# Optimization experiments

Hardware: AMD Instinct MI355X
Metric: run time of the kernel (lower is better)

## Reference

```python
import jax, jax.numpy as jnp
import numpy as np

N = 102400          # total nodes
G = 64              # graphs
S = 16              # subgraphs per graph
NODES_PER_SG = 100  # nodes per subgraph (N = G*S*NODES_PER_SG)
D = 128             # in_dim == emb_dim
L = 5               # num_layer
E = 819200          # edges (avg degree 8)
TOTAL_SG = G * S    # total subgraphs = 1024 (static)


def setup_inputs() -> dict:
    key = jax.random.key(0)
    kx, ke, kw1, kw2, keps = jax.random.split(key, 5)
    x = jax.random.normal(kx, (N, D), dtype=jnp.float32)
    edge_index = jax.random.randint(ke, (2, E), 0, N, dtype=jnp.int32)
    # node -> graph id (contiguous blocks of S*NODES_PER_SG nodes)
    batch = (jnp.arange(N, dtype=jnp.int32) // (S * NODES_PER_SG)).astype(jnp.int32)
    # node -> local subgraph id within its graph
    subgraph_batch = ((jnp.arange(N, dtype=jnp.int32) // NODES_PER_SG) % S).astype(jnp.int32)
    num_subgraphs = jnp.full((G,), S, dtype=jnp.int32)
    # GIN MLP params per layer: Linear(D,2D) -> ReLU -> Linear(2D,D)
    s1 = 1.0 / np.sqrt(D)
    s2 = 1.0 / np.sqrt(2 * D)
    W1 = jax.random.normal(kw1, (L, D, 2 * D), dtype=jnp.float32) * s1
    b1 = jnp.zeros((L, 2 * D), dtype=jnp.float32)
    W2 = jax.random.normal(kw2, (L, 2 * D, D), dtype=jnp.float32) * s2
    b2 = jnp.zeros((L, D), dtype=jnp.float32)
    eps = jnp.zeros((L,), dtype=jnp.float32)
    return {"x": x, "edge_index": edge_index, "batch": batch,
            "subgraph_batch": subgraph_batch, "num_subgraphs": num_subgraphs,
            "W1": W1, "b1": b1, "W2": W2, "b2": b2, "eps": eps}


def reference(x, edge_index, batch, subgraph_batch, num_subgraphs, W1, b1, W2, b2, eps):
    src, dst = edge_index[0], edge_index[1]
    n = x.shape[0]
    h = x
    for i in range(L):
        # GIN aggregation: (1+eps)*h + sum over incoming messages
        agg = jax.ops.segment_sum(h[src], dst, num_segments=n)
        z = (1.0 + eps[i]) * h + agg
        z = jax.nn.relu(z @ W1[i] + b1[i]) @ W2[i] + b2[i]
        h = z if i == L - 1 else jax.nn.relu(z)  # inter-layer ReLU, JK='last'
    # subgraph_pool: global subgraph index = graph offset + local subgraph id
    tmp = jnp.concatenate([jnp.zeros((1,), num_subgraphs.dtype),
                           jnp.cumsum(num_subgraphs)])
    subgraph_idx = tmp[batch] + subgraph_batch  # [N], values in [0, TOTAL_SG)
    sums = jax.ops.segment_sum(h, subgraph_idx, num_segments=TOTAL_SG)
    cnt = jax.ops.segment_sum(jnp.ones((n, 1), h.dtype), subgraph_idx,
                              num_segments=TOTAL_SG)
    return sums / jnp.maximum(cnt, 1.0)  # global_mean_pool over subgraphs
```

## Files before the change

kernel.cpp:

```cpp
#include <hip/hip_runtime.h>
#include <cstddef>

#define NN   102400
#define D    128
#define D2   256
#define NE   819200
#define NL   5
#define NSG  1024
#define SGN  100

typedef __attribute__((ext_vector_type(8))) short short8;
typedef __attribute__((ext_vector_type(4))) float f32x4;

__device__ __forceinline__ float bf2f(unsigned short u) {
  union { unsigned int i; float f; } c; c.i = ((unsigned int)u) << 16; return c.f;
}
__device__ __forceinline__ unsigned short f2bf(float f) {
  union { float f; unsigned int i; } c; c.f = f;
  unsigned int x = c.i;
  return (unsigned short)((x + 0x7fffu + ((x >> 16) & 1u)) >> 16);
}

__global__ void k_count(const int* __restrict__ dst, int* __restrict__ deg,
                        int* __restrict__ rank) {
  int e = blockIdx.x * blockDim.x + threadIdx.x;
  if (e < NE) rank[e] = atomicAdd(&deg[dst[e]], 1);
}

__global__ void k_scan_local(const int* __restrict__ deg, int* __restrict__ incl,
                             int* __restrict__ part) {
  __shared__ int s[1024];
  int i = blockIdx.x * 1024 + threadIdx.x;
  s[threadIdx.x] = deg[i];
  __syncthreads();
  for (int off = 1; off < 1024; off <<= 1) {
    int t = (threadIdx.x >= off) ? s[threadIdx.x - off] : 0;
    __syncthreads();
    s[threadIdx.x] += t;
    __syncthreads();
  }
  incl[i] = s[threadIdx.x];
  if (threadIdx.x == 1023) part[blockIdx.x] = s[1023];
}

__global__ void k_scan_part(int* part, int nb) {
  if (threadIdx.x == 0 && blockIdx.x == 0) {
    int acc = 0;
    for (int i = 0; i < nb; ++i) { int t = part[i]; part[i] = acc; acc += t; }
  }
}

__global__ void k_scan_fin(const int* __restrict__ incl, const int* __restrict__ part,
                           int* __restrict__ rowptr) {
  int i = blockIdx.x * blockDim.x + threadIdx.x;
  if (i < NN) rowptr[i + 1] = incl[i] + part[i >> 10];
  if (i == 0) rowptr[0] = 0;
}

__global__ void k_fill(const int* __restrict__ src, const int* __restrict__ dst,
                       const int* __restrict__ rowptr, const int* __restrict__ rank,
                       int* __restrict__ csrsrc) {
  int e = blockIdx.x * blockDim.x + threadIdx.x;
  if (e < NE) csrsrc[rowptr[dst[e]] + rank[e]] = src[e];
}

__global__ void k_cvt_x(const float* __restrict__ x, unsigned short* __restrict__ xb) {
  int i = blockIdx.x * 256 + threadIdx.x;
  const float* p = x + (size_t)i * 8;
  float4 a = *(const float4*)p;
  float4 b = *(const float4*)(p + 4);
  short8 o;
  o[0] = (short)f2bf(a.x); o[1] = (short)f2bf(a.y);
  o[2] = (short)f2bf(a.z); o[3] = (short)f2bf(a.w);
  o[4] = (short)f2bf(b.x); o[5] = (short)f2bf(b.y);
  o[6] = (short)f2bf(b.z); o[7] = (short)f2bf(b.w);
  *(short8*)(xb + (size_t)i * 8) = o;
}

__global__ void k_prep_w(const float* __restrict__ W1, const float* __restrict__ W2,
                         unsigned short* __restrict__ W1t, unsigned short* __restrict__ W2t) {
  int i = blockIdx.x * 256 + threadIdx.x;
  int l = i >> 15;
  int rem = i & 32767;
  int n1 = rem >> 7, k1 = rem & 127;
  W1t[i] = f2bf(W1[(size_t)l * D * D2 + (size_t)k1 * D2 + n1]);
  int n2 = rem >> 8, k2 = rem & 255;
  W2t[i] = f2bf(W2[(size_t)l * D2 * D + (size_t)k2 * D + n2]);
}

template<bool RELU_OUT>
__global__ __launch_bounds__(256, 2) void k_layer(
    const unsigned short* __restrict__ hin, const int* __restrict__ rowptr,
    const int* __restrict__ csrsrc,
    const unsigned short* __restrict__ W1t,
    const float* __restrict__ b1,
    const unsigned short* __restrict__ W2t,
    const float* __restrict__ b2,
    const float* __restrict__ eps, int layer,
    unsigned short* __restrict__ hout) {
  __shared__ char lds[4 * 4096];
  int w = threadIdx.x >> 6, lane = threadIdx.x & 63;
  int l15 = lane & 15, q = lane >> 4;
  char* my = lds + w * 4096;
  float ep1 = 1.0f + eps[layer];
  int rowA = blockIdx.x * 128 + w * 32;

  short8 azf[2][4];
#pragma unroll
  for (int m = 0; m < 2; ++m) {
    int r = rowA + m * 16 + l15;
    const unsigned short* hr = hin + (size_t)r * D + q * 8;
    float acc[4][8];
#pragma unroll
    for (int kf = 0; kf < 4; ++kf) {
      short8 v = *(const short8*)(hr + kf * 32);
#pragma unroll
      for (int j = 0; j < 8; ++j) acc[kf][j] = ep1 * bf2f((unsigned short)v[j]);
    }
    int e0 = rowptr[r], e1 = rowptr[r + 1];
    for (int e = e0; e < e1; ++e) {
      int u = csrsrc[e];
      const unsigned short* hu = hin + (size_t)u * D + q * 8;
#pragma unroll
      for (int kf = 0; kf < 4; ++kf) {
        short8 v = *(const short8*)(hu + kf * 32);
#pragma unroll
        for (int j = 0; j < 8; ++j) acc[kf][j] += bf2f((unsigned short)v[j]);
      }
    }
#pragma unroll
    for (int kf = 0; kf < 4; ++kf) {
      short8 o;
#pragma unroll
      for (int j = 0; j < 8; ++j) o[j] = (short)f2bf(acc[kf][j]);
      azf[m][kf] = o;
    }
  }

  f32x4 acc2[2][8] = {};
#pragma unroll
  for (int nc = 0; nc < 4; ++nc) {
    f32x4 acc1[2][4] = {};
#pragma unroll
    for (int kf = 0; kf < 4; ++kf) {
#pragma unroll
      for (int n = 0; n < 4; ++n) {
        int col = nc * 64 + n * 16 + l15;
        short8 bf = *(const short8*)(W1t + (size_t)col * D + kf * 32 + q * 8);
        acc1[0][n] = __builtin_amdgcn_mfma_f32_16x16x32_bf16(azf[0][kf], bf, acc1[0][n], 0, 0, 0);
        acc1[1][n] = __builtin_amdgcn_mfma_f32_16x16x32_bf16(azf[1][kf], bf, acc1[1][n], 0, 0, 0);
      }
    }
#pragma unroll
    for (int m = 0; m < 2; ++m) {
#pragma unroll
      for (int n = 0; n < 4; ++n) {
        int cc = n * 16 + l15;
        float bb = b1[nc * 64 + cc];
#pragma unroll
        for (int r = 0; r < 4; ++r) {
          int rs = m * 16 + q * 4 + r;
          float v = fmaxf(acc1[m][n][r] + bb, 0.f);
          int byte = (rs << 7) + cc * 2;
          byte ^= (rs & 7) << 4;
          *(unsigned short*)(my + byte) = f2bf(v);
        }
      }
    }
#pragma unroll
    for (int kk = 0; kk < 2; ++kk) {
      short8 af[2];
#pragma unroll
      for (int m = 0; m < 2; ++m) {
        int rs = m * 16 + l15;
        int byte = (rs << 7) + kk * 64 + q * 16;
        byte ^= (rs & 7) << 4;
        af[m] = *(const short8*)(my + byte);
      }
#pragma unroll
      for (int n2 = 0; n2 < 8; ++n2) {
        short8 bf = *(const short8*)(W2t + (size_t)(n2 * 16 + l15) * D2 +
                                     nc * 64 + kk * 32 + q * 8);
        acc2[0][n2] = __builtin_amdgcn_mfma_f32_16x16x32_bf16(af[0], bf, acc2[0][n2], 0, 0, 0);
        acc2[1][n2] = __builtin_amdgcn_mfma_f32_16x16x32_bf16(af[1], bf, acc2[1][n2], 0, 0, 0);
      }
    }
  }

#pragma unroll
  for (int m = 0; m < 2; ++m) {
#pragma unroll
    for (int n2 = 0; n2 < 8; ++n2) {
      int col = n2 * 16 + l15;
      float bb = b2[col];
#pragma unroll
      for (int r = 0; r < 4; ++r) {
        int row = rowA + m * 16 + q * 4 + r;
        float v = acc2[m][n2][r] + bb;
        if (RELU_OUT) v = fmaxf(v, 0.f);
        hout[(size_t)row * D + col] = f2bf(v);
      }
    }
  }
}

__global__ __launch_bounds__(256) void k_pool(const unsigned short* __restrict__ h,
                                              float* __restrict__ out) {
  __shared__ float red[16][132];
  int g = threadIdx.x >> 4;
  int ln = threadIdx.x & 15;
  int sg = blockIdx.x;
  float acc[8] = {0.f, 0.f, 0.f, 0.f, 0.f, 0.f, 0.f, 0.f};
  for (int r = g; r < SGN; r += 16) {
    short8 v = *(const short8*)(h + ((size_t)sg * SGN + r) * D + (size_t)ln * 8);
#pragma unroll
    for (int j = 0; j < 8; ++j) acc[j] += bf2f((unsigned short)v[j]);
  }
#pragma unroll
  for (int j = 0; j < 8; ++j) red[g][ln * 8 + j] = acc[j];
  __syncthreads();
  if (threadIdx.x < 128) {
    float s = 0.f;
#pragma unroll
    for (int i = 0; i < 16; ++i) s += red[i][threadIdx.x];
    out[(size_t)sg * D + threadIdx.x] = s * 0.01f;
  }
}

extern "C" void kernel_launch(void* const* d_in, const int* in_sizes, int n_in,
                              void* d_out, int out_size, void* d_ws, size_t ws_size,
                              hipStream_t stream) {
  const float* x   = (const float*)d_in[0];
  const int*   ei  = (const int*)d_in[1];
  const float* W1  = (const float*)d_in[5];
  const float* b1  = (const float*)d_in[6];
  const float* W2  = (const float*)d_in[7];
  const float* b2  = (const float*)d_in[8];
  const float* eps = (const float*)d_in[9];
  const int* src = ei;
  const int* dst = ei + NE;

  char* p = (char*)d_ws;
  unsigned short* xb  = (unsigned short*)p; p += (size_t)NN * D * 2;
  unsigned short* hb  = (unsigned short*)p; p += (size_t)NN * D * 2;
  unsigned short* zb  = (unsigned short*)p; p += (size_t)NN * D * 2;
  unsigned short* W1t = (unsigned short*)p; p += (size_t)NL * D * D2 * 2;
  unsigned short* W2t = (unsigned short*)p; p += (size_t)NL * D * D2 * 2;
  int* deg    = (int*)p;   p += (size_t)NN * 4;
  int* incl   = (int*)p;   p += (size_t)NN * 4;
  int* part   = (int*)p;   p += 128 * 4;
  int* rowptr = (int*)p;   p += (size_t)(NN + 1) * 4;
  int* rank   = (int*)p;   p += (size_t)NE * 4;
  int* csrsrc = (int*)p;   p += (size_t)NE * 4;

  hipMemsetAsync(deg, 0, (size_t)NN * 4, stream);
  k_count<<<NE / 256, 256, 0, stream>>>(dst, deg, rank);
  k_scan_local<<<NN / 1024, 1024, 0, stream>>>(deg, incl, part);
  k_scan_part<<<1, 64, 0, stream>>>(part, NN / 1024);
  k_scan_fin<<<NN / 256, 256, 0, stream>>>(incl, part, rowptr);
  k_fill<<<NE / 256, 256, 0, stream>>>(src, dst, rowptr, rank, csrsrc);

  k_cvt_x<<<NN * D / 8 / 256, 256, 0, stream>>>(x, xb);
  k_prep_w<<<NL * D * D2 / 256, 256, 0, stream>>>(W1, W2, W1t, W2t);

  const unsigned short* cur = xb;
  unsigned short* nxt = hb;
  for (int l = 0; l < NL; ++l) {
    const unsigned short* w1l = W1t + (size_t)l * D * D2;
    const unsigned short* w2l = W2t + (size_t)l * D * D2;
    const float* b1l = b1 + (size_t)l * D2;
    const float* b2l = b2 + (size_t)l * D;
    if (l < NL - 1)
      k_layer<true><<<NN / 128, 256, 0, stream>>>(cur, rowptr, csrsrc, w1l, b1l,
                                                  w2l, b2l, eps, l, nxt);
    else
      k_layer<false><<<NN / 128, 256, 0, stream>>>(cur, rowptr, csrsrc, w1l, b1l,
                                                   w2l, b2l, eps, l, nxt);
    cur = nxt;
    nxt = (cur == hb) ? zb : hb;
  }
  k_pool<<<NSG, 256, 0, stream>>>((const unsigned short*)cur, (float*)d_out);
}
```

Before: 745.6 us.

## Split neighbor aggregation into a separate high-parallelism kernel before the MLP

Neighbor aggregation moves out of the fused layer kernel into its own kernel. Each node gets 16 threads, one 16-byte slice each, and the edge loop is unrolled by four so more gathers are in flight. The MLP kernel then just loads the aggregated bf16 rows. This is meant to fix the poor memory-level parallelism of the fused gather, where the MFMA-oriented thread layout and the register pressure of launch_bounds(256,2) limited outstanding loads. In exchange it adds an extra write and read of an N×D bf16 buffer per layer plus one extra launch per layer.

```diff
diff --git a/kernel.cpp b/kernel.cpp
--- a/kernel.cpp
+++ b/kernel.cpp
@@ -88,54 +88,67 @@
   W2t[i] = f2bf(W2[(size_t)l * D2 * D + (size_t)k2 * D + n2]);
 }
 
+__global__ __launch_bounds__(256) void k_agg(const unsigned short* __restrict__ h,
+                                             const int* __restrict__ rowptr,
+                                             const int* __restrict__ csrsrc,
+                                             const float* __restrict__ eps, int layer,
+                                             unsigned short* __restrict__ z) {
+  int g = threadIdx.x >> 4;
+  int ln = threadIdx.x & 15;
+  int v = blockIdx.x * 16 + g;
+  float ep1 = 1.0f + eps[layer];
+  const size_t off = (size_t)ln * 8;
+
+  short8 hv = *(const short8*)(h + (size_t)v * D + off);
+  float acc[8];
+#pragma unroll
+  for (int j = 0; j < 8; ++j) acc[j] = ep1 * bf2f((unsigned short)hv[j]);
+
+  int e = rowptr[v], r1 = rowptr[v + 1];
+  for (; e + 3 < r1; e += 4) {
+    int u0 = csrsrc[e], u1 = csrsrc[e + 1], u2 = csrsrc[e + 2], u3 = csrsrc[e + 3];
+    short8 a = *(const short8*)(h + (size_t)u0 * D + off);
+    short8 b = *(const short8*)(h + (size_t)u1 * D + off);
+    short8 c = *(const short8*)(h + (size_t)u2 * D + off);
+    short8 d = *(const short8*)(h + (size_t)u3 * D + off);
+#pragma unroll
+    for (int j = 0; j < 8; ++j)
+      acc[j] += (bf2f((unsigned short)a[j]) + bf2f((unsigned short)b[j])) +
+                (bf2f((unsigned short)c[j]) + bf2f((unsigned short)d[j]));
+  }
+  for (; e < r1; ++e) {
+    int u0 = csrsrc[e];
+    short8 a = *(const short8*)(h + (size_t)u0 * D + off);
+#pragma unroll
+    for (int j = 0; j < 8; ++j) acc[j] += bf2f((unsigned short)a[j]);
+  }
+
+  short8 o;
+#pragma unroll
+  for (int j = 0; j < 8; ++j) o[j] = (short)f2bf(acc[j]);
+  *(short8*)(z + (size_t)v * D + off) = o;
+}
+
 template<bool RELU_OUT>
-__global__ __launch_bounds__(256, 2) void k_layer(
-    const unsigned short* __restrict__ hin, const int* __restrict__ rowptr,
-    const int* __restrict__ csrsrc,
+__global__ __launch_bounds__(256, 2) void k_mlp(
+    const unsigned short* __restrict__ z,
     const unsigned short* __restrict__ W1t,
     const float* __restrict__ b1,
     const unsigned short* __restrict__ W2t,
     const float* __restrict__ b2,
-    const float* __restrict__ eps, int layer,
     unsigned short* __restrict__ hout) {
   __shared__ char lds[4 * 4096];
   int w = threadIdx.x >> 6, lane = threadIdx.x & 63;
   int l15 = lane & 15, q = lane >> 4;
   char* my = lds + w * 4096;
-  float ep1 = 1.0f + eps[layer];
   int rowA = blockIdx.x * 128 + w * 32;
 
   short8 azf[2][4];
 #pragma unroll
-  for (int m = 0; m < 2; ++m) {
-    int r = rowA + m * 16 + l15;
-    const unsigned short* hr = hin + (size_t)r * D + q * 8;
-    float acc[4][8];
-#pragma unroll
-    for (int kf = 0; kf < 4; ++kf) {
-      short8 v = *(const short8*)(hr + kf * 32);
-#pragma unroll
-      for (int j = 0; j < 8; ++j) acc[kf][j] = ep1 * bf2f((unsigned short)v[j]);
-    }
-    int e0 = rowptr[r], e1 = rowptr[r + 1];
-    for (int e = e0; e < e1; ++e) {
-      int u = csrsrc[e];
-      const unsigned short* hu = hin + (size_t)u * D + q * 8;
-#pragma unroll
-      for (int kf = 0; kf < 4; ++kf) {
-        short8 v = *(const short8*)(hu + kf * 32);
-#pragma unroll
-        for (int j = 0; j < 8; ++j) acc[kf][j] += bf2f((unsigned short)v[j]);
-      }
-    }
-#pragma unroll
-    for (int kf = 0; kf < 4; ++kf) {
-      short8 o;
-#pragma unroll
-      for (int j = 0; j < 8; ++j) o[j] = (short)f2bf(acc[kf][j]);
-      azf[m][kf] = o;
-    }
-  }
+  for (int m = 0; m < 2; ++m)
+#pragma unroll
+    for (int kf = 0; kf < 4; ++kf)
+      azf[m][kf] = *(const short8*)(z + (size_t)(rowA + m * 16 + l15) * D + kf * 32 + q * 8);
 
   f32x4 acc2[2][8] = {};
 #pragma unroll
@@ -244,6 +257,7 @@
   unsigned short* xb  = (unsigned short*)p; p += (size_t)NN * D * 2;
   unsigned short* hb  = (unsigned short*)p; p += (size_t)NN * D * 2;
   unsigned short* zb  = (unsigned short*)p; p += (size_t)NN * D * 2;
+  unsigned short* ga  = (unsigned short*)p; p += (size_t)NN * D * 2;
   unsigned short* W1t = (unsigned short*)p; p += (size_t)NL * D * D2 * 2;
   unsigned short* W2t = (unsigned short*)p; p += (size_t)NL * D * D2 * 2;
   int* deg    = (int*)p;   p += (size_t)NN * 4;
@@ -270,12 +284,11 @@
     const unsigned short* w2l = W2t + (size_t)l * D * D2;
     const float* b1l = b1 + (size_t)l * D2;
     const float* b2l = b2 + (size_t)l * D;
+    k_agg<<<NN / 16, 256, 0, stream>>>(cur, rowptr, csrsrc, eps, l, ga);
     if (l < NL - 1)
-      k_layer<true><<<NN / 128, 256, 0, stream>>>(cur, rowptr, csrsrc, w1l, b1l,
-                                                  w2l, b2l, eps, l, nxt);
+      k_mlp<true><<<NN / 128, 256, 0, stream>>>(ga, w1l, b1l, w2l, b2l, nxt);
     else
-      k_layer<false><<<NN / 128, 256, 0, stream>>>(cur, rowptr, csrsrc, w1l, b1l,
-                                                   w2l, b2l, eps, l, nxt);
+      k_mlp<false><<<NN / 128, 256, 0, stream>>>(ga, w1l, b1l, w2l, b2l, nxt);
     cur = nxt;
     nxt = (cur == hb) ? zb : hb;
   }
```

Measured after the change: 702.5 us. 1.06x faster.
